# Kernel tuning notes

Hardware: AMD Instinct MI355X
Metric: run time of the kernel (lower is better)

The kernel has to match this reference:

```python
import jax, jax.numpy as jnp
import numpy as np
from jax import lax

B, S, H, E, K = 2, 1024, 2048, 16, 4
CAP = int(B * S * 1.5 * K / E)  # capacity = 768
ALPHA = 0.7

def _mlp2(x, w1, b1, w2, b2):
    return jnp.maximum(x @ w1 + b1, 0.0) @ w2 + b2

def setup_inputs() -> dict:
    key = jax.random.key(0)
    ks = iter(jax.random.split(key, 32))
    def w(shape, scale=0.02):
        return (jax.random.normal(next(ks), shape, dtype=jnp.float32) * scale)
    inp = {
        'hidden_states': jax.random.normal(next(ks), (B, S, H), dtype=jnp.float32),
        'mod_image': jax.random.normal(next(ks), (B, S, H), dtype=jnp.float32),
        'mod_genomic': jax.random.normal(next(ks), (B, S, H), dtype=jnp.float32),
        'g_w1': w((H, H)), 'g_b1': jnp.zeros((H,), jnp.float32),
        'g_w2': w((H, E)), 'g_b2': jnp.zeros((E,), jnp.float32),
        'm_w1': w((H, H)), 'm_b1': jnp.zeros((H,), jnp.float32),
        'm_w2': w((H, H)), 'm_b2': jnp.zeros((H,), jnp.float32),
    }
    for p in ('si', 'sg', 'sc', 'sb'):
        inp[p + '_w1'] = w((H, H // 2)); inp[p + '_b1'] = jnp.zeros((H // 2,), jnp.float32)
        inp[p + '_w2'] = w((H // 2, E)); inp[p + '_b2'] = jnp.zeros((E,), jnp.float32)
    return inp

def reference(hidden_states, mod_image, mod_genomic,
              g_w1, g_b1, g_w2, g_b2,
              si_w1, si_b1, si_w2, si_b2,
              sg_w1, sg_b1, sg_w2, sg_b2,
              sc_w1, sc_b1, sc_w2, sc_b2,
              sb_w1, sb_b1, sb_w2, sb_b2,
              m_w1, m_b1, m_w2, m_b2):
    # generalized router probs over experts
    g_probs = jax.nn.softmax(_mlp2(hidden_states, g_w1, g_b1, g_w2, g_b2), axis=-1)
    # missing-modality representation (clinical + biospecimen are missing)
    miss = _mlp2(hidden_states, m_w1, m_b1, m_w2, m_b2)
    # specialized routers: image, genomic (available) + clinical, biospecimen (use miss)
    s_probs = (jax.nn.softmax(_mlp2(mod_image, si_w1, si_b1, si_w2, si_b2), axis=-1)
               + jax.nn.softmax(_mlp2(mod_genomic, sg_w1, sg_b1, sg_w2, sg_b2), axis=-1)
               + jax.nn.softmax(_mlp2(miss, sc_w1, sc_b1, sc_w2, sc_b2), axis=-1)
               + jax.nn.softmax(_mlp2(miss, sb_w1, sb_b1, sb_w2, sb_b2), axis=-1))
    s_probs = s_probs / 2.0  # divided by len(available_modalities) == 2, as in source
    router_probs = ALPHA * g_probs + (1.0 - ALPHA) * s_probs  # [B,S,E]
    top_k_probs, top_k_idx = lax.top_k(router_probs, K)  # [B,S,K]
    top_k_probs = top_k_probs / top_k_probs.sum(axis=-1, keepdims=True)
    onehot = jax.nn.one_hot(top_k_idx, E, dtype=router_probs.dtype)  # [B,S,K,E]
    dmask = onehot.sum(axis=-2)                               # [B,S,E] (0/1: experts distinct)
    cmask = (onehot * top_k_probs[..., None]).sum(axis=-2)    # [B,S,E]
    dispatch = jnp.zeros((B, S, E, CAP), router_probs.dtype).at[..., 0].set(dmask)
    combine = jnp.zeros((B, S, E, CAP), router_probs.dtype).at[..., 0].set(cmask)
    mean_probs = router_probs.mean(axis=(0, 1))  # [E]
    aux_loss = jnp.sum(mean_probs * jnp.log(mean_probs * E + 1e-9))
    return dispatch, combine, router_probs, aux_loss
```

## Files before the change

kernel.cpp:

```cpp
#include <hip/hip_runtime.h>
#include <math.h>
#include <stdint.h>

#define NTOK 2048
#define HDIM 2048
#define HHALF 1024
#define EDIM 16
#define CAPV 768
#define TOPK 4
#define GK 2048

typedef __bf16 bf16x8 __attribute__((ext_vector_type(8)));
typedef __bf16 bf16x4 __attribute__((ext_vector_type(4)));
typedef float f32x4 __attribute__((ext_vector_type(4)));


struct GJobA {
  const __bf16 *Ah, *Al, *Wh, *Wl;
  const float* bias;
  float* Cf; __bf16 *Ch, *Cl;
  int relu, N, blk0;
};
struct GJobsA { GJobA j[6]; };

#define BKA 32
#define NTA 64

#define BARR __builtin_amdgcn_s_barrier()
#define LGKM0 do { asm volatile("s_waitcnt lgkmcnt(0)" ::: "memory"); \
                   __builtin_amdgcn_sched_barrier(0); } while (0)
#define PRIO1 __builtin_amdgcn_s_setprio(1)
#define PRIO0 __builtin_amdgcn_s_setprio(0)

__global__ __launch_bounds__(512, 2) void gemm_phased(GJobsA P) {
  __shared__ __align__(16) __bf16 lds[2][4][256 * BKA];

  const int tid = threadIdx.x;
  const int wid = tid >> 6, lane = tid & 63;
  const int lane15 = lane & 15, c0 = lane >> 4;

  const int bid = blockIdx.x;
  int ji = 0;
#pragma unroll
  for (int k = 1; k < 6; ++k)
    if (bid >= P.j[k].blk0) ji = k;
  const GJobA J = P.j[ji];
  const int local = bid - J.blk0;
  const int nbx = J.N >> 8;
  const int bx = local & (nbx - 1);
  const int by = local / nbx;
  const int m0 = by * 256, n0 = bx * 256;

  const int wr = wid >> 2, wc = wid & 3;

  int srow[2], soff[2];
#pragma unroll
  for (int h = 0; h < 2; ++h) {
    int s = tid + h * 512;
    int row = s >> 2;
    srow[h] = row;
    soff[h] = ((s & 3) ^ ((row >> 1) & 3)) * 8;
  }

  int offB[4], offA[2][4];
#pragma unroll
  for (int ni = 0; ni < 4; ++ni) {
    int rb = wc * 64 + ni * 16 + lane15;
    offB[ni] = rb * 64 + ((c0 ^ ((rb >> 1) & 3)) << 4);
  }
#pragma unroll
  for (int mh = 0; mh < 2; ++mh)
#pragma unroll
    for (int i = 0; i < 4; ++i) {
      int ra = wr * 128 + mh * 64 + i * 16 + lane15;
      offA[mh][i] = ra * 64 + ((c0 ^ ((ra >> 1) & 3)) << 4);
    }

#define STAGE2(gptr, grow0, k1, larr)                                          \
  { _Pragma("unroll") for (int h = 0; h < 2; ++h) {                            \
      const __bf16* _src =                                                     \
          (gptr) + (size_t)((grow0) + srow[h]) * GK + (k1) + soff[h];          \
      __builtin_amdgcn_global_load_lds(                                        \
          (const __attribute__((address_space(1))) uint32_t*)_src,             \
          (__attribute__((address_space(3))) uint32_t*)((larr) +               \
              (wid * 64 + h * 512) * 8), 16, 0, 0); } }

#define DSR_A(dst, base, h)                                                    \
  { _Pragma("unroll") for (int i = 0; i < 4; ++i)                              \
      dst[i] = *(const bf16x8*)((base) + offA[h][i]); }
#define DSR_B(dst, base)                                                       \
  { _Pragma("unroll") for (int i = 0; i < 4; ++i)                              \
      dst[i] = *(const bf16x8*)((base) + offB[i]); }
#define MFMA16(af, bf, mh)                                                     \
  { _Pragma("unroll") for (int mi = 0; mi < 4; ++mi)                           \
    _Pragma("unroll") for (int ni = 0; ni < 4; ++ni)                           \
      acc[(mh) * 4 + mi][ni] = __builtin_amdgcn_mfma_f32_16x16x32_bf16(        \
          af[mi], bf[ni], acc[(mh) * 4 + mi][ni], 0, 0, 0); }

  f32x4 acc[8][4];
#pragma unroll
  for (int i = 0; i < 8; ++i)
#pragma unroll
    for (int j = 0; j < 4; ++j) acc[i][j] = (f32x4){0.f, 0.f, 0.f, 0.f};

  STAGE2(J.Ah, m0, 0, lds[0][0]);
  STAGE2(J.Wh, n0, 0, lds[0][2]);
  STAGE2(J.Wl, n0, 0, lds[0][3]);
  STAGE2(J.Al, m0, 0, lds[0][1]);
  asm volatile("s_waitcnt vmcnt(2)" ::: "memory");
  BARR;

  bf16x8 ah[4], al[4], bh[4], bl[4];

  for (int t = 0; t < NTA; ++t) {
    const int cur = t & 1, nxt = cur ^ 1;
    const bool hasNext = (t + 1 < NTA);
    const int k1 = (t + 1) * BKA;
    const char* cAh = (const char*)lds[cur][0];
    const char* cAl = (const char*)lds[cur][1];
    const char* cBh = (const char*)lds[cur][2];
    const char* cBl = (const char*)lds[cur][3];

    DSR_A(ah, cAh, 0);
    DSR_B(bh, cBh);
    DSR_B(bl, cBl);
    if (hasNext) STAGE2(J.Ah, m0, k1, lds[nxt][0]);
    BARR; LGKM0;
    PRIO1; MFMA16(ah, bh, 0); MFMA16(ah, bl, 0); PRIO0;
    if (hasNext) { asm volatile("s_waitcnt vmcnt(2)" ::: "memory"); }
    else         { asm volatile("s_waitcnt vmcnt(0)" ::: "memory"); }
    BARR;
    DSR_A(al, cAl, 0);
    DSR_A(ah, cAh, 1);
    if (hasNext) {
      STAGE2(J.Wh, n0, k1, lds[nxt][2]);
      STAGE2(J.Wl, n0, k1, lds[nxt][3]);
      STAGE2(J.Al, m0, k1, lds[nxt][1]);
    }
    BARR; LGKM0;
    PRIO1; MFMA16(al, bh, 0); MFMA16(ah, bh, 1); PRIO0;
    BARR;
    DSR_A(al, cAl, 1);
    BARR; LGKM0;
    PRIO1; MFMA16(ah, bl, 1); MFMA16(al, bh, 1); PRIO0;
    if (hasNext) { asm volatile("s_waitcnt vmcnt(2)" ::: "memory"); }
    BARR;
  }

#pragma unroll
  for (int mh = 0; mh < 2; ++mh)
#pragma unroll
    for (int mi = 0; mi < 4; ++mi)
#pragma unroll
      for (int ni = 0; ni < 4; ++ni) {
        int col = n0 + wc * 64 + ni * 16 + lane15;
        float bv = J.bias[col];
        f32x4 v = acc[mh * 4 + mi][ni];
#pragma unroll
        for (int j = 0; j < 4; ++j) {
          int row = m0 + wr * 128 + mh * 64 + mi * 16 + c0 * 4 + j;
          float x = v[j] + bv;
          if (J.relu) x = fmaxf(x, 0.0f);
          size_t o = (size_t)row * J.N + col;
          if (J.Cf) J.Cf[o] = x;
          if (J.Ch) {
            __bf16 hh = (__bf16)x;
            J.Ch[o] = hh;
            J.Cl[o] = (__bf16)(x - (float)hh);
          }
        }
      }
#undef STAGE2
#undef DSR_A
#undef DSR_B
#undef MFMA16
}

#define BKT 64

struct GJob {
  const __bf16* Ah; const __bf16* Al;
  const __bf16* Wh; const __bf16* Wl;
  const float* bias;
  float* Cf;
  __bf16* Ch; __bf16* Cl;
  int relu; int N; int blk0; int kLen;
};
struct GJobs { GJob j[4]; int njobs; };

__device__ __forceinline__ void stage_tile(const __bf16* __restrict__ g,
                                           int grow0, int k0,
                                           __bf16* lbase, int wid, int lane) {
  int r_in = lane >> 3;
  int swz_elems = ((lane & 7) ^ r_in) << 3;
#pragma unroll
  for (int i = 0; i < 4; ++i) {
    int row0 = wid * 32 + i * 8;
    const __bf16* src = g + (size_t)(grow0 + row0 + r_in) * GK + k0 + swz_elems;
    __builtin_amdgcn_global_load_lds(
        (const __attribute__((address_space(1))) uint32_t*)src,
        (__attribute__((address_space(3))) uint32_t*)(lbase + row0 * BKT),
        16, 0, 0);
  }
}

__global__ __launch_bounds__(256) void gemm_split(GJobs P) {
  __shared__ __align__(16) __bf16 lds[4 * 128 * BKT];
  __bf16* ldsAh = lds;
  __bf16* ldsAl = lds + 8192;
  __bf16* ldsBh = lds + 16384;
  __bf16* ldsBl = lds + 24576;
  const char* cAh = (const char*)ldsAh;
  const char* cAl = (const char*)ldsAl;
  const char* cBh = (const char*)ldsBh;
  const char* cBl = (const char*)ldsBl;

  const int bid = blockIdx.x;
  int ji = 0;
#pragma unroll
  for (int k = 1; k < 4; ++k)
    if (k < P.njobs && bid >= P.j[k].blk0) ji = k;
  const GJob J = P.j[ji];
  const int local = bid - J.blk0;
  const int nbx = J.N >> 7;
  const int bx = local & (nbx - 1);
  const int by = local / nbx;
  const int m0 = by * 128;
  const int n0 = bx * 128;

  const int tid = threadIdx.x;
  const int wid = tid >> 6;
  const int lane = tid & 63;
  const int lane15 = lane & 15;
  const int c0 = lane >> 4;
  const int wr = wid >> 1;
  const int wc = wid & 1;

  int offA[4][2], offB[4][2];
#pragma unroll
  for (int i = 0; i < 4; ++i) {
    int ra = wr * 64 + i * 16 + lane15;
    int rb = wc * 64 + i * 16 + lane15;
#pragma unroll
    for (int ks = 0; ks < 2; ++ks) {
      offA[i][ks] = ra * 128 + (((ks * 4 + c0) ^ (ra & 7)) << 4);
      offB[i][ks] = rb * 128 + (((ks * 4 + c0) ^ (rb & 7)) << 4);
    }
  }

  f32x4 acc[4][4];
#pragma unroll
  for (int i = 0; i < 4; ++i)
#pragma unroll
    for (int j = 0; j < 4; ++j) acc[i][j] = (f32x4){0.f, 0.f, 0.f, 0.f};

  for (int k0 = 0; k0 < J.kLen; k0 += BKT) {
    stage_tile(J.Ah, m0, k0, ldsAh, wid, lane);
    stage_tile(J.Al, m0, k0, ldsAl, wid, lane);
    stage_tile(J.Wh, n0, k0, ldsBh, wid, lane);
    stage_tile(J.Wl, n0, k0, ldsBl, wid, lane);
    __syncthreads();
#pragma unroll
    for (int ks = 0; ks < 2; ++ks) {
      bf16x8 ah[4], al[4], bh[4], bl[4];
#pragma unroll
      for (int i = 0; i < 4; ++i) {
        ah[i] = *(const bf16x8*)(cAh + offA[i][ks]);
        al[i] = *(const bf16x8*)(cAl + offA[i][ks]);
        bh[i] = *(const bf16x8*)(cBh + offB[i][ks]);
        bl[i] = *(const bf16x8*)(cBl + offB[i][ks]);
      }
#pragma unroll
      for (int mi = 0; mi < 4; ++mi)
#pragma unroll
        for (int ni = 0; ni < 4; ++ni) {
          acc[mi][ni] = __builtin_amdgcn_mfma_f32_16x16x32_bf16(
              ah[mi], bh[ni], acc[mi][ni], 0, 0, 0);
          acc[mi][ni] = __builtin_amdgcn_mfma_f32_16x16x32_bf16(
              ah[mi], bl[ni], acc[mi][ni], 0, 0, 0);
          acc[mi][ni] = __builtin_amdgcn_mfma_f32_16x16x32_bf16(
              al[mi], bh[ni], acc[mi][ni], 0, 0, 0);
        }
    }
    __syncthreads();
  }

#pragma unroll
  for (int mi = 0; mi < 4; ++mi) {
#pragma unroll
    for (int ni = 0; ni < 4; ++ni) {
      int col = n0 + wc * 64 + ni * 16 + lane15;
      float bv = J.bias[col];
      f32x4 v = acc[mi][ni];
#pragma unroll
      for (int j = 0; j < 4; ++j) {
        int row = m0 + wr * 64 + mi * 16 + c0 * 4 + j;
        float x = v[j] + bv;
        if (J.relu) x = fmaxf(x, 0.0f);
        size_t o = (size_t)row * J.N + col;
        if (J.Cf) J.Cf[o] = x;
        if (J.Ch) {
          __bf16 hh = (__bf16)x;
          J.Ch[o] = hh;
          J.Cl[o] = (__bf16)(x - (float)hh);
        }
      }
    }
  }
}

struct SJob { const float* in; __bf16* h; __bf16* l; };
struct TJob { const float* W; __bf16* Th; __bf16* Tl; int Nd; };
struct PrepArgs {
  SJob s[4];
  TJob t[6];
  const float* pb2;
  const float* pW1a; const float* pb1a; float* pva;
  const float* pW1b; const float* pb1b; float* pvb;
};

__global__ __launch_bounds__(256) void prep(PrepArgs P) {
  __shared__ float tbuf[32][33];
  const int bid = blockIdx.x;
  const int tid = threadIdx.x;
  if (bid < 16384) {
    SJob J = P.s[bid >> 12];
    int i = (bid & 4095) * 256 + tid;
    float4 v = ((const float4*)J.in)[i];
    bf16x4 hv, lv;
    hv.x = (__bf16)v.x; lv.x = (__bf16)(v.x - (float)hv.x);
    hv.y = (__bf16)v.y; lv.y = (__bf16)(v.y - (float)hv.y);
    hv.z = (__bf16)v.z; lv.z = (__bf16)(v.z - (float)hv.z);
    hv.w = (__bf16)v.w; lv.w = (__bf16)(v.w - (float)hv.w);
    ((bf16x4*)J.h)[i] = hv;
    ((bf16x4*)J.l)[i] = lv;
  } else if (bid < 32768) {
    int local = bid - 16384;
    int ji, ln;
    if (local < 4096)      { ji = 0; ln = local; }
    else if (local < 8192) { ji = 1; ln = local - 4096; }
    else { ji = 2 + ((local - 8192) >> 11); ln = (local - 8192) & 2047; }
    TJob J = P.t[ji];
    int full = (J.Nd == HDIM);
    int n0 = (full ? (ln & 63) : (ln & 31)) * 32;
    int k0 = (full ? (ln >> 6) : (ln >> 5)) * 32;
    int tx = tid & 31, ty = tid >> 5;
#pragma unroll
    for (int i = 0; i < 4; ++i) {
      int kk = ty + i * 8;
      tbuf[kk][tx] = J.W[(size_t)(k0 + kk) * J.Nd + n0 + tx];
    }
    __syncthreads();
#pragma unroll
    for (int i = 0; i < 4; ++i) {
      int nn = ty + i * 8;
      float v = tbuf[tx][nn];
      __bf16 hh = (__bf16)v;
      size_t o = (size_t)(n0 + nn) * GK + k0 + tx;
      J.Th[o] = hh;
      J.Tl[o] = (__bf16)(v - (float)hh);
    }
  } else {
    int local = bid - 32768;
    int side = local >> 5; int r = local & 31;
    const float* W1 = side ? P.pW1b : P.pW1a;
    const float* b1 = side ? P.pb1b : P.pb1a;
    float* v = side ? P.pvb : P.pva;
    int n = (r & 3) * 256 + tid;
    int k0 = (r >> 2) * 256;
    float acc = (k0 == 0) ? b1[n] : 0.0f;
#pragma unroll 8
    for (int k = 0; k < 256; ++k)
      acc = fmaf(P.pb2[k0 + k], W1[(size_t)(k0 + k) * HHALF + n], acc);
    atomicAdd(&v[n], acc);
  }
}

struct LJob { const float* Y; const float* Y2; const float* W2;
              const float* b2; float* L; int K; int relu; };
struct LJobs { LJob j[5]; };
__global__ __launch_bounds__(256) void logits_kernel(LJobs P) {
  const LJob J = P.j[blockIdx.x >> 8];
  const int blk = blockIdx.x & 255;
  const int tid = threadIdx.x;
  const int wid = tid >> 6, lane = tid & 63;
  const int e = lane & 15;
  const int kq = lane >> 4;
  const int tok0 = blk * 8 + wid * 2;
  const float* y0 = J.Y + (size_t)tok0 * J.K;
  const float* y1 = y0 + J.K;
  const float* z0 = J.Y2 + (size_t)tok0 * J.K;
  const float* z1 = z0 + J.K;
  const int KQ = J.K >> 2;
  const int kbase = kq * KQ;
  float a0 = 0.f, a1 = 0.f;
  if (J.relu) {
#pragma unroll 8
    for (int k = 0; k < KQ; ++k) {
      int kk = kbase + k;
      float w = J.W2[(size_t)kk * EDIM + e];
      float v0 = fmaxf(y0[kk] + z0[kk], 0.0f);
      float v1 = fmaxf(y1[kk] + z1[kk], 0.0f);
      a0 = fmaf(v0, w, a0);
      a1 = fmaf(v1, w, a1);
    }
  } else {
#pragma unroll 8
    for (int k = 0; k < KQ; ++k) {
      int kk = kbase + k;
      float w = J.W2[(size_t)kk * EDIM + e];
      a0 = fmaf(y0[kk], w, a0);
      a1 = fmaf(y1[kk], w, a1);
    }
  }
  a0 += __shfl_xor(a0, 16); a0 += __shfl_xor(a0, 32);
  a1 += __shfl_xor(a1, 16); a1 += __shfl_xor(a1, 32);
  if (lane < 16) {
    float b = J.b2[e];
    J.L[(size_t)tok0 * EDIM + e] = a0 + b;
    J.L[(size_t)(tok0 + 1) * EDIM + e] = a1 + b;
  }
}

__device__ __forceinline__ void softmax16(const float* __restrict__ L, float* __restrict__ p) {
  float v[16];
  *(float4*)&v[0]  = *(const float4*)&L[0];
  *(float4*)&v[4]  = *(const float4*)&L[4];
  *(float4*)&v[8]  = *(const float4*)&L[8];
  *(float4*)&v[12] = *(const float4*)&L[12];
  float m = v[0];
#pragma unroll
  for (int e = 1; e < 16; ++e) m = fmaxf(m, v[e]);
  float s = 0.0f;
#pragma unroll
  for (int e = 0; e < 16; ++e) { v[e] = expf(v[e] - m); s += v[e]; }
  float inv = 1.0f / s;
#pragma unroll
  for (int e = 0; e < 16; ++e) p[e] = v[e] * inv;
}

__global__ __launch_bounds__(256) void finalize_kernel(
    const float* __restrict__ Lg, const float* __restrict__ Lsi,
    const float* __restrict__ Lsg, const float* __restrict__ Lsc,
    const float* __restrict__ Lsb,
    float* __restrict__ dispatch, float* __restrict__ combine,
    float* __restrict__ router_probs, float* __restrict__ mean_acc) {
  __shared__ float sm[EDIM];
  int tid = threadIdx.x;
  if (tid < EDIM) sm[tid] = 0.0f;
  __syncthreads();

  int tok = blockIdx.x * 256 + tid;
  float pg[16], ps[16], tmp[16], r[16];
  softmax16(Lg + (size_t)tok * EDIM, pg);
  softmax16(Lsi + (size_t)tok * EDIM, ps);
  softmax16(Lsg + (size_t)tok * EDIM, tmp);
#pragma unroll
  for (int e = 0; e < 16; ++e) ps[e] += tmp[e];
  softmax16(Lsc + (size_t)tok * EDIM, tmp);
#pragma unroll
  for (int e = 0; e < 16; ++e) ps[e] += tmp[e];
  softmax16(Lsb + (size_t)tok * EDIM, tmp);
#pragma unroll
  for (int e = 0; e < 16; ++e) ps[e] += tmp[e];

#pragma unroll
  for (int e = 0; e < 16; ++e) {
    float s = ps[e] * 0.5f;
    r[e] = 0.7f * pg[e] + 0.3f * s;
  }

#pragma unroll
  for (int e = 0; e < 16; e += 4) {
    float4 o = {r[e], r[e + 1], r[e + 2], r[e + 3]};
    *(float4*)&router_probs[(size_t)tok * EDIM + e] = o;
  }

#pragma unroll
  for (int e = 0; e < 16; ++e) atomicAdd(&sm[e], r[e]);

  bool used[16];
#pragma unroll
  for (int e = 0; e < 16; ++e) used[e] = false;
  int idx[TOPK];
  float tp[TOPK];
  float tsum = 0.0f;
#pragma unroll
  for (int j = 0; j < TOPK; ++j) {
    float best = -1.0f;
    int bi = 0;
#pragma unroll
    for (int e = 0; e < 16; ++e) {
      bool take = (!used[e]) && (r[e] > best);
      best = take ? r[e] : best;
      bi = take ? e : bi;
    }
    used[bi] = true;
    idx[j] = bi;
    tp[j] = best;
    tsum += best;
  }
  float invt = 1.0f / tsum;
#pragma unroll
  for (int j = 0; j < TOPK; ++j) {
    size_t off = ((size_t)tok * EDIM + idx[j]) * CAPV;
    dispatch[off] = 1.0f;
    combine[off] = tp[j] * invt;
  }

  __syncthreads();
  if (tid < EDIM) atomicAdd(&mean_acc[tid], sm[tid]);
}

__global__ void aux_kernel(const float* __restrict__ mean_acc, float* __restrict__ out_aux) {
  if (threadIdx.x == 0 && blockIdx.x == 0) {
    float s = 0.0f;
    for (int e = 0; e < EDIM; ++e) {
      float m = mean_acc[e] * (1.0f / (float)NTOK);
      s += m * logf(m * (float)EDIM + 1e-9f);
    }
    *out_aux = s;
  }
}

#define MBYTE (1ull << 20)

extern "C" void kernel_launch(void* const* d_in, const int* in_sizes, int n_in,
                              void* d_out, int out_size, void* d_ws, size_t ws_size,
                              hipStream_t stream) {
  const float* X    = (const float*)d_in[0];
  const float* IMG  = (const float*)d_in[1];
  const float* GEN  = (const float*)d_in[2];
  const float* g_w1 = (const float*)d_in[3];
  const float* g_b1 = (const float*)d_in[4];
  const float* g_w2 = (const float*)d_in[5];
  const float* g_b2 = (const float*)d_in[6];
  const float* m_w1 = (const float*)d_in[7];
  const float* m_b1 = (const float*)d_in[8];
  const float* m_w2 = (const float*)d_in[9];
  const float* m_b2 = (const float*)d_in[10];
  const float* si_w1 = (const float*)d_in[11];
  const float* si_b1 = (const float*)d_in[12];
  const float* si_w2 = (const float*)d_in[13];
  const float* si_b2 = (const float*)d_in[14];
  const float* sg_w1 = (const float*)d_in[15];
  const float* sg_b1 = (const float*)d_in[16];
  const float* sg_w2 = (const float*)d_in[17];
  const float* sg_b2 = (const float*)d_in[18];
  const float* sc_w1 = (const float*)d_in[19];
  const float* sc_b1 = (const float*)d_in[20];
  const float* sc_w2 = (const float*)d_in[21];
  const float* sc_b2 = (const float*)d_in[22];
  const float* sb_w1 = (const float*)d_in[23];
  const float* sb_b1 = (const float*)d_in[24];
  const float* sb_w2 = (const float*)d_in[25];
  const float* sb_b2 = (const float*)d_in[26];

  char* wsb = (char*)d_ws;
  __bf16* Xh    = (__bf16*)(wsb + 0 * MBYTE);
  __bf16* Xl    = (__bf16*)(wsb + 8 * MBYTE);
  __bf16* IMGh  = (__bf16*)(wsb + 16 * MBYTE);
  __bf16* IMGl  = (__bf16*)(wsb + 24 * MBYTE);
  __bf16* GENh  = (__bf16*)(wsb + 32 * MBYTE);
  __bf16* GENl  = (__bf16*)(wsb + 40 * MBYTE);
  __bf16* M2h   = (__bf16*)(wsb + 48 * MBYTE);
  __bf16* M2l   = (__bf16*)(wsb + 56 * MBYTE);
  __bf16* Wm1h  = (__bf16*)(wsb + 64 * MBYTE);
  __bf16* Wm1l  = (__bf16*)(wsb + 72 * MBYTE);
  __bf16* Wg1h  = (__bf16*)(wsb + 80 * MBYTE);
  __bf16* Wg1l  = (__bf16*)(wsb + 88 * MBYTE);
  __bf16* Wsch  = (__bf16*)(wsb + 96 * MBYTE);
  __bf16* Wscl  = (__bf16*)(wsb + 100 * MBYTE);
  __bf16* Wsbh  = (__bf16*)(wsb + 104 * MBYTE);
  __bf16* Wsbl  = (__bf16*)(wsb + 108 * MBYTE);
  __bf16* Wsih  = (__bf16*)(wsb + 112 * MBYTE);
  __bf16* Wsil  = (__bf16*)(wsb + 116 * MBYTE);
  __bf16* Wsgh  = (__bf16*)(wsb + 120 * MBYTE);
  __bf16* Wsgl  = (__bf16*)(wsb + 124 * MBYTE);
  __bf16* H1h   = (__bf16*)(wsb + 128 * MBYTE);
  __bf16* H1l   = (__bf16*)(wsb + 136 * MBYTE);
  __bf16* WPsch = (__bf16*)(wsb + 144 * MBYTE);
  __bf16* WPscl = (__bf16*)(wsb + 148 * MBYTE);
  __bf16* WPsbh = (__bf16*)(wsb + 152 * MBYTE);
  __bf16* WPsbl = (__bf16*)(wsb + 156 * MBYTE);
  float*  YG    = (float*)(wsb + 160 * MBYTE);
  float*  YSI   = (float*)(wsb + 176 * MBYTE);
  float*  YSG   = (float*)(wsb + 184 * MBYTE);
  float*  YSCp0 = (float*)(wsb + 192 * MBYTE);
  float*  YSCp1 = (float*)(wsb + 200 * MBYTE);
  float*  YSBp0 = (float*)(wsb + 208 * MBYTE);
  float*  YSBp1 = (float*)(wsb + 216 * MBYTE);
  float* L0 = (float*)(wsb + 224 * MBYTE);
  float* L1 = L0 + NTOK * EDIM;
  float* L2 = L1 + NTOK * EDIM;
  float* L3 = L2 + NTOK * EDIM;
  float* L4 = L3 + NTOK * EDIM;
  float* meanp = L4 + NTOK * EDIM;
  float* zbias = meanp + EDIM;
  float* vsc = zbias + GK;
  float* vsb = vsc + HHALF;

  float* dispatch = (float*)d_out;
  float* combine = dispatch + (size_t)NTOK * EDIM * CAPV;
  float* rp = combine + (size_t)NTOK * EDIM * CAPV;
  float* aux = rp + (size_t)NTOK * EDIM;

  hipMemsetAsync(d_out, 0, (size_t)out_size * sizeof(float), stream);
  hipMemsetAsync(meanp, 0, (EDIM + GK + 2 * HHALF) * sizeof(float), stream);

  dim3 blk(256);

  {
    PrepArgs p;
    p.s[0] = {X, Xh, Xl};
    p.s[1] = {IMG, IMGh, IMGl};
    p.s[2] = {GEN, GENh, GENl};
    p.s[3] = {m_w2, M2h, M2l};
    p.t[0] = {m_w1, Wm1h, Wm1l, HDIM};
    p.t[1] = {g_w1, Wg1h, Wg1l, HDIM};
    p.t[2] = {sc_w1, Wsch, Wscl, HHALF};
    p.t[3] = {sb_w1, Wsbh, Wsbl, HHALF};
    p.t[4] = {si_w1, Wsih, Wsil, HHALF};
    p.t[5] = {sg_w1, Wsgh, Wsgl, HHALF};
    p.pb2 = m_b2;
    p.pW1a = sc_w1; p.pb1a = sc_b1; p.pva = vsc;
    p.pW1b = sb_w1; p.pb1b = sb_b1; p.pvb = vsb;
    prep<<<32832, blk, 0, stream>>>(p);
  }

  {
    GJobsA g;
    g.j[0] = {Xh, Xl, Wm1h, Wm1l, m_b1, nullptr, H1h, H1l, 1, HDIM, 0};
    g.j[1] = {Xh, Xl, Wg1h, Wg1l, g_b1, YG, nullptr, nullptr, 1, HDIM, 64};
    g.j[2] = {IMGh, IMGl, Wsih, Wsil, si_b1, YSI, nullptr, nullptr, 1, HHALF, 128};
    g.j[3] = {GENh, GENl, Wsgh, Wsgl, sg_b1, YSG, nullptr, nullptr, 1, HHALF, 160};
    g.j[4] = {Wsch, Wscl, M2h, M2l, zbias, nullptr, WPsch, WPscl, 0, HDIM, 192};
    g.j[5] = {Wsbh, Wsbl, M2h, M2l, zbias, nullptr, WPsbh, WPsbl, 0, HDIM, 224};
    gemm_phased<<<256, dim3(512), 0, stream>>>(g);
  }

  {
    GJobs g;
    g.j[0] = {H1h, H1l, WPsch, WPscl, vsc, YSCp0, nullptr, nullptr, 0, HHALF, 0, 1024};
    g.j[1] = {H1h + 1024, H1l + 1024, WPsch + 1024, WPscl + 1024, zbias, YSCp1,
              nullptr, nullptr, 0, HHALF, 128, 1024};
    g.j[2] = {H1h, H1l, WPsbh, WPsbl, vsb, YSBp0, nullptr, nullptr, 0, HHALF, 256, 1024};
    g.j[3] = {H1h + 1024, H1l + 1024, WPsbh + 1024, WPsbl + 1024, zbias, YSBp1,
              nullptr, nullptr, 0, HHALF, 384, 1024};
    g.njobs = 4;
    gemm_split<<<512, blk, 0, stream>>>(g);
  }

  {
    LJobs l;
    l.j[0] = {YG, YG, g_w2, g_b2, L0, HDIM, 0};
    l.j[1] = {YSI, YSI, si_w2, si_b2, L1, HHALF, 0};
    l.j[2] = {YSG, YSG, sg_w2, sg_b2, L2, HHALF, 0};
    l.j[3] = {YSCp0, YSCp1, sc_w2, sc_b2, L3, HHALF, 1};
    l.j[4] = {YSBp0, YSBp1, sb_w2, sb_b2, L4, HHALF, 1};
    logits_kernel<<<5 * 256, blk, 0, stream>>>(l);
  }

  finalize_kernel<<<NTOK / 256, blk, 0, stream>>>(L0, L1, L2, L3, L4,
                                                  dispatch, combine, rp, meanp);
  aux_kernel<<<1, 64, 0, stream>>>(meanp, aux);
}
```

Measured before the change: 405.8 us.

## Replace phased split-bf16 GEMM with 4-slot ring pipeline over unrolled K passes

The split-precision GEMM (hi/lo parts of A and W) is restructured from a double-buffered loop that loaded four tiles per step into a 4-slot LDS ring. It runs 192 sequential steps: Ah*Wh, then Ah*Wl, then Al*Wh, each over 64 K-tiles, keeping three stages in flight. The goal is deeper prefetch and less waiting on global loads per barrier. The same number of MFMAs remains, but there are more barriers, and the A tiles are reloaded in each of the three passes, which raises global traffic.

```diff
diff --git a/kernel.cpp b/kernel.cpp
--- a/kernel.cpp
+++ b/kernel.cpp
@@ -24,7 +24,7 @@
 struct GJobsA { GJobA j[6]; };
 
 #define BKA 32
-#define NTA 64
+#define NTR 192
 
 #define BARR __builtin_amdgcn_s_barrier()
 #define LGKM0 do { asm volatile("s_waitcnt lgkmcnt(0)" ::: "memory"); \
@@ -32,8 +32,8 @@
 #define PRIO1 __builtin_amdgcn_s_setprio(1)
 #define PRIO0 __builtin_amdgcn_s_setprio(0)
 
-__global__ __launch_bounds__(512, 2) void gemm_phased(GJobsA P) {
-  __shared__ __align__(16) __bf16 lds[2][4][256 * BKA];
+__global__ __launch_bounds__(512, 2) void gemm_ring(GJobsA P) {
+  __shared__ __align__(16) __bf16 lds[4][2][256 * BKA];
 
   const int tid = threadIdx.x;
   const int wid = tid >> 6, lane = tid & 63;
@@ -84,6 +84,13 @@
           (const __attribute__((address_space(1))) uint32_t*)_src,             \
           (__attribute__((address_space(3))) uint32_t*)((larr) +               \
               (wid * 64 + h * 512) * 8), 16, 0, 0); } }
+
+#define STAGE_A(tt)                                                            \
+  { const __bf16* _as = ((tt) >= 128) ? J.Al : J.Ah;                           \
+    STAGE2(_as, m0, ((tt) & 63) * BKA, lds[(tt) & 3][0]); }
+#define STAGE_B(tt)                                                            \
+  { const __bf16* _bs = (((tt) >= 64) && ((tt) < 128)) ? J.Wl : J.Wh;          \
+    STAGE2(_bs, n0, ((tt) & 63) * BKA, lds[(tt) & 3][1]); }
 
 #define DSR_A(dst, base, h)                                                    \
   { _Pragma("unroll") for (int i = 0; i < 4; ++i)                              \
@@ -103,47 +110,32 @@
 #pragma unroll
     for (int j = 0; j < 4; ++j) acc[i][j] = (f32x4){0.f, 0.f, 0.f, 0.f};
 
-  STAGE2(J.Ah, m0, 0, lds[0][0]);
-  STAGE2(J.Wh, n0, 0, lds[0][2]);
-  STAGE2(J.Wl, n0, 0, lds[0][3]);
-  STAGE2(J.Al, m0, 0, lds[0][1]);
-  asm volatile("s_waitcnt vmcnt(2)" ::: "memory");
+  STAGE_A(0); STAGE_B(0);
+  STAGE_A(1); STAGE_B(1);
+  STAGE_A(2); STAGE_B(2);
+  asm volatile("s_waitcnt vmcnt(8)" ::: "memory");
   BARR;
 
-  bf16x8 ah[4], al[4], bh[4], bl[4];
-
-  for (int t = 0; t < NTA; ++t) {
-    const int cur = t & 1, nxt = cur ^ 1;
-    const bool hasNext = (t + 1 < NTA);
-    const int k1 = (t + 1) * BKA;
-    const char* cAh = (const char*)lds[cur][0];
-    const char* cAl = (const char*)lds[cur][1];
-    const char* cBh = (const char*)lds[cur][2];
-    const char* cBl = (const char*)lds[cur][3];
-
-    DSR_A(ah, cAh, 0);
-    DSR_B(bh, cBh);
-    DSR_B(bl, cBl);
-    if (hasNext) STAGE2(J.Ah, m0, k1, lds[nxt][0]);
+  bf16x8 a[4], b[4];
+
+  for (int t = 0; t < NTR; ++t) {
+    const char* cA = (const char*)lds[t & 3][0];
+    const char* cB = (const char*)lds[t & 3][1];
+    const bool st = (t + 3 < NTR);
+
+    DSR_A(a, cA, 0);
+    DSR_B(b, cB);
+    if (st) STAGE_A(t + 3);
     BARR; LGKM0;
-    PRIO1; MFMA16(ah, bh, 0); MFMA16(ah, bl, 0); PRIO0;
-    if (hasNext) { asm volatile("s_waitcnt vmcnt(2)" ::: "memory"); }
-    else         { asm volatile("s_waitcnt vmcnt(0)" ::: "memory"); }
+    PRIO1; MFMA16(a, b, 0); PRIO0;
     BARR;
-    DSR_A(al, cAl, 0);
-    DSR_A(ah, cAh, 1);
-    if (hasNext) {
-      STAGE2(J.Wh, n0, k1, lds[nxt][2]);
-      STAGE2(J.Wl, n0, k1, lds[nxt][3]);
-      STAGE2(J.Al, m0, k1, lds[nxt][1]);
-    }
+    DSR_A(a, cA, 1);
+    if (st) STAGE_B(t + 3);
     BARR; LGKM0;
-    PRIO1; MFMA16(al, bh, 0); MFMA16(ah, bh, 1); PRIO0;
-    BARR;
-    DSR_A(al, cAl, 1);
-    BARR; LGKM0;
-    PRIO1; MFMA16(ah, bl, 1); MFMA16(al, bh, 1); PRIO0;
-    if (hasNext) { asm volatile("s_waitcnt vmcnt(2)" ::: "memory"); }
+    PRIO1; MFMA16(a, b, 1); PRIO0;
+    if (t < NTR - 3)       { asm volatile("s_waitcnt vmcnt(8)" ::: "memory"); }
+    else if (t == NTR - 3) { asm volatile("s_waitcnt vmcnt(4)" ::: "memory"); }
+    else if (t == NTR - 2) { asm volatile("s_waitcnt vmcnt(0)" ::: "memory"); }
     BARR;
   }
 
@@ -171,6 +163,8 @@
         }
       }
 #undef STAGE2
+#undef STAGE_A
+#undef STAGE_B
 #undef DSR_A
 #undef DSR_B
 #undef MFMA16
@@ -636,7 +630,7 @@
     g.j[3] = {GENh, GENl, Wsgh, Wsgl, sg_b1, YSG, nullptr, nullptr, 1, HHALF, 160};
     g.j[4] = {Wsch, Wscl, M2h, M2l, zbias, nullptr, WPsch, WPscl, 0, HDIM, 192};
     g.j[5] = {Wsbh, Wsbl, M2h, M2l, zbias, nullptr, WPsbh, WPsbl, 0, HDIM, 224};
-    gemm_phased<<<256, dim3(512), 0, stream>>>(g);
+    gemm_ring<<<256, dim3(512), 0, stream>>>(g);
   }
 
   {
```

Measured after the change: 429.9 us. 1.06x slower.
